# Optimization experiments

Hardware: AMD Instinct MI355X
Metric: run time of the kernel (lower is better)

Reference implementation:

```python
import jax, jax.numpy as jnp
import numpy as np

N = 50000      # nodes / stations
E = 600000     # edges
IN = 16        # in_channels
ED = 8         # edge_dim
HID = 128      # hidden
H = 4          # heads
C = HID // H   # 32 per-head channels
EMB = HID // 2 # station embedding dim
FEAT = HID - EMB
SLOPE = 0.2    # GATv2 LeakyReLU negative slope


def setup_inputs() -> dict:
    key = jax.random.key(0)
    ks = jax.random.split(key, 32)
    r = lambda i, shape, s=0.05: (jax.random.normal(ks[i], shape, jnp.float32) * s)
    inp = {
        "x": jax.random.normal(ks[0], (N, IN), jnp.float32),
        "node_idx": jax.random.randint(ks[1], (N,), 0, N),
        "edge_index": jax.random.randint(ks[2], (2, E), 0, N),
        "edge_attr": jax.random.normal(ks[3], (E, ED), jnp.float32),
        # params
        "emb": r(4, (N, EMB)),
        "W_in": r(5, (IN, FEAT)), "b_in": jnp.zeros((FEAT,), jnp.float32),
        # conv1 (GATv2: lin_l, lin_r, lin_edge, att, out bias)
        "Wl1": r(6, (HID, HID)), "bl1": jnp.zeros((HID,), jnp.float32),
        "Wr1": r(7, (HID, HID)), "br1": jnp.zeros((HID,), jnp.float32),
        "We1": r(8, (ED, HID)),  "be1": jnp.zeros((HID,), jnp.float32),
        "att1": r(9, (H, C)),    "bo1": jnp.zeros((HID,), jnp.float32),
        # conv2
        "Wl2": r(10, (HID, HID)), "bl2": jnp.zeros((HID,), jnp.float32),
        "Wr2": r(11, (HID, HID)), "br2": jnp.zeros((HID,), jnp.float32),
        "We2": r(12, (ED, HID)),  "be2": jnp.zeros((HID,), jnp.float32),
        "att2": r(13, (H, C)),    "bo2": jnp.zeros((HID,), jnp.float32),
        # layer norms
        "g1": jnp.ones((HID,), jnp.float32), "beta1": jnp.zeros((HID,), jnp.float32),
        "g2": jnp.ones((HID,), jnp.float32), "beta2": jnp.zeros((HID,), jnp.float32),
        # output head
        "W_out": r(14, (HID, 1)), "b_out": jnp.zeros((1,), jnp.float32),
    }
    return inp


def _gatv2(x, src, dst, ea, Wl, bl, Wr, br, We, be, att, bo):
    # x: [N,HID] -> per-head projections [N,H,C]
    xl = (x @ Wl + bl).reshape(-1, H, C)   # source transform
    xr = (x @ Wr + br).reshape(-1, H, C)   # target transform
    ee = (ea @ We + be).reshape(-1, H, C)  # edge transform [E,H,C]
    s = jax.nn.leaky_relu(xl[src] + xr[dst] + ee, SLOPE)  # [E,H,C]
    logit = jnp.einsum('ehc,hc->eh', s, att)              # [E,H]
    # segment softmax over destination node
    amax = jax.lax.stop_gradient(jax.ops.segment_max(logit, dst, num_segments=N))
    amax = jnp.where(jnp.isfinite(amax), amax, 0.0)
    ex = jnp.exp(logit - amax[dst])
    den = jax.ops.segment_sum(ex, dst, num_segments=N)
    alpha = ex / den[dst]                                  # [E,H]
    out = jax.ops.segment_sum(xl[src] * alpha[..., None], dst, num_segments=N)
    return out.reshape(-1, HID) + bo


def _ln(x, g, b):
    mu = x.mean(-1, keepdims=True)
    v = ((x - mu) ** 2).mean(-1, keepdims=True)
    return (x - mu) * jax.lax.rsqrt(v + 1e-5) * g + b


def reference(x, node_idx, edge_index, edge_attr, emb, W_in, b_in,
              Wl1, bl1, Wr1, br1, We1, be1, att1, bo1,
              Wl2, bl2, Wr2, br2, We2, be2, att2, bo2,
              g1, beta1, g2, beta2, W_out, b_out):
    src, dst = edge_index[0], edge_index[1]
    feat = jax.nn.relu(x @ W_in + b_in)                       # [N,FEAT]
    z = jnp.concatenate([feat, emb[node_idx]], axis=-1)       # [N,HID]
    h = jax.nn.relu(_gatv2(z, src, dst, edge_attr, Wl1, bl1, Wr1, br1, We1, be1, att1, bo1))
    z = _ln(z + h, g1, beta1)
    h = jax.nn.relu(_gatv2(z, src, dst, edge_attr, Wl2, bl2, Wr2, br2, We2, be2, att2, bo2))
    z = _ln(z + h, g2, beta2)
    return (z @ W_out + b_out).squeeze(-1)                    # [N]
```

## Files before the change

kernel.cpp:

```cpp
#include <hip/hip_runtime.h>
#include <hip/hip_bf16.h>

#define NN 50000
#define NE 600000
#define IND 16
#define EDD 8
#define HIDD 128
#define NH 4
#define CC 32
#define EMBD 64
#define FEATD 64
#define NB_SCAN ((NN + 255) / 256)
#define FILLB ((NE + 255) / 256)
#define BZB (NN / 16)
#define WPB 256
#define PRMF 896

typedef __hip_bfloat16 bf16;
typedef __attribute__((ext_vector_type(8))) short bshort8;
typedef __attribute__((ext_vector_type(4))) float floatx4;
typedef __attribute__((ext_vector_type(2))) float f32x2;

__device__ __forceinline__ unsigned short f2bu(float f) {
    unsigned int u = __float_as_uint(f);
    u += 0x7fffu + ((u >> 16) & 1u);
    return (unsigned short)(u >> 16);
}

#if defined(__has_builtin)
#if __has_builtin(__builtin_amdgcn_fdot2_f32_bf16)
#define HAS_DOT2BF 1
#endif
#endif
#ifndef HAS_DOT2BF
#define HAS_DOT2BF 0
#endif

#if HAS_DOT2BF
typedef __attribute__((ext_vector_type(2))) __bf16 bfx2;
__device__ __forceinline__ float dot2bf(unsigned int a, unsigned int b, float c) {
    return __builtin_amdgcn_fdot2_f32_bf16(__builtin_bit_cast(bfx2, a),
                                           __builtin_bit_cast(bfx2, b), c, false);
}
#else
__device__ __forceinline__ float dot2bf(unsigned int a, unsigned int b, float c) {
    float a0 = __uint_as_float(a << 16), a1 = __uint_as_float(a & 0xffff0000u);
    float b0 = __uint_as_float(b << 16), b1 = __uint_as_float(b & 0xffff0000u);
    return __builtin_fmaf(a1, b1, __builtin_fmaf(a0, b0, c));
}
#endif

template <bool F32>
__device__ __forceinline__ float LD(const void* p, long long i) {
    if constexpr (F32) return ((const float*)p)[i];
    else return __bfloat162float(((const bf16*)p)[i]);
}

__device__ __forceinline__ bool is_f32(const int* cnt) { return *cnt > 8; }

__global__ void k_detinit(const unsigned short* __restrict__ x, int nhalf,
                          int* __restrict__ cnt, int* __restrict__ deg,
                          int* __restrict__ dcnt) {
    if (blockIdx.x == 0) {
        __shared__ int red[256];
        int hits = 0;
        for (int i = threadIdx.x; i < nhalf; i += 256)
            if ((x[i] & 0x7F80u) == 0x7F80u) hits++;
        red[threadIdx.x] = hits;
        __syncthreads();
        for (int o = 128; o; o >>= 1) {
            if (threadIdx.x < o) red[threadIdx.x] += red[threadIdx.x + o];
            __syncthreads();
        }
        if (threadIdx.x == 0) *cnt = red[0];
    } else {
        int gid = (blockIdx.x - 1) * 256 + threadIdx.x;
        if (gid < NN) deg[gid] = 0;
        if (blockIdx.x == 1 && threadIdx.x < 64) dcnt[threadIdx.x] = 0;
    }
}

__global__ void k_hist(const int* __restrict__ ei, int* __restrict__ deg, int* __restrict__ rank) {
    int e = blockIdx.x * blockDim.x + threadIdx.x;
    if (e < NE) rank[e] = atomicAdd(&deg[ei[NE + e]], 1);
}

__global__ void k_scan1(const int* __restrict__ deg, int* __restrict__ off0,
                        int* __restrict__ bsum, int* __restrict__ dcnt,
                        int* __restrict__ rankd) {
    __shared__ int tile[256];
    __shared__ int lh[64];
    __shared__ int lbase[64];
    int t = threadIdx.x;
    int gid = blockIdx.x * 256 + t;
    if (t < 64) lh[t] = 0;
    __syncthreads();
    int v = (gid < NN) ? deg[gid] : 0;
    int b = 63 - min(v, 63);
    int lr = 0;
    if (gid < NN) lr = atomicAdd(&lh[b], 1);
    tile[t] = v;
    __syncthreads();
    if (t < 64) lbase[t] = lh[t] ? atomicAdd(&dcnt[t], lh[t]) : 0;
    #pragma unroll
    for (int o = 1; o < 256; o <<= 1) {
        int u = (t >= o) ? tile[t - o] : 0;
        __syncthreads();
        tile[t] += u;
        __syncthreads();
    }
    if (gid < NN) {
        off0[gid] = tile[t] - v;
        rankd[gid] = lbase[b] + lr;
    }
    if (t == 255) bsum[blockIdx.x] = tile[255];
}
__global__ void k_scan2(int* __restrict__ bsum, int* __restrict__ dcnt,
                        int* __restrict__ dbase) {
    __shared__ int tile[256];
    __shared__ int d2[64];
    int t = threadIdx.x;
    int v = (t < NB_SCAN) ? bsum[t] : 0;
    tile[t] = v;
    int dv = (t < 64) ? dcnt[t] : 0;
    if (t < 64) d2[t] = dv;
    __syncthreads();
    #pragma unroll
    for (int o = 1; o < 256; o <<= 1) {
        int u = (t >= o) ? tile[t - o] : 0;
        __syncthreads();
        tile[t] += u;
        __syncthreads();
    }
    #pragma unroll
    for (int o = 1; o < 64; o <<= 1) {
        int u = (t >= o && t < 64) ? d2[t - o] : 0;
        __syncthreads();
        if (t < 64) d2[t] += u;
        __syncthreads();
    }
    if (t < NB_SCAN) bsum[t] = tile[t] - v;
    if (t < 64) dbase[t] = d2[t] - dv;
}

template <bool F32>
__device__ void prep_impl(const int* __restrict__ off0, const int* __restrict__ bsum,
                          const int* __restrict__ deg, const int* __restrict__ rankd,
                          const int* __restrict__ dbase, int* __restrict__ perm,
                          int* __restrict__ offF,
                          const int* __restrict__ ei, const int* __restrict__ rank,
                          int* __restrict__ esrc, uint4* __restrict__ ea8, const void* ea,
                          const void* x, const int* __restrict__ node_idx, const void* emb,
                          const void* W_in, const void* b_in, bf16* __restrict__ zb,
                          const void* Wl1, const void* bl1, const void* Wr1, const void* br1,
                          const void* Wl2, const void* bl2, const void* Wr2, const void* br2,
                          bf16* __restrict__ wbT, float* __restrict__ bias,
                          const void* We1, const void* att1, const void* be1, const void* bo1,
                          const void* g1, const void* beta1,
                          const void* We2, const void* att2, const void* be2, const void* bo2,
                          const void* g2, const void* beta2,
                          const void* Wo, const void* bout,
                          unsigned int* __restrict__ wep, float* __restrict__ prm) {
    int b = blockIdx.x;
    int t = threadIdx.x;
    if (b < NB_SCAN) {
        int gid = b * 256 + t;
        if (gid < NN) {
            offF[gid] = off0[gid] + bsum[b];
            int bk = 63 - min(deg[gid], 63);
            perm[dbase[bk] + rankd[gid]] = gid;
        }
        if (gid == 0) offF[NN] = NE;
    } else if (b < NB_SCAN + FILLB) {
        int e = (b - NB_SCAN) * 256 + t;
        if (e >= NE) return;
        if (e < 16) {
            esrc[NE + e] = 0;
            uint4 z; z.x = 0; z.y = 0; z.z = 0; z.w = 0;
            ea8[NE + e] = z;
        }
        int dst = ei[NE + e];
        int slot = off0[dst] + bsum[dst >> 8] + rank[e];
        esrc[slot] = ei[e];
        uint4 v;
        if constexpr (F32) {
            const float4* ef = (const float4*)ea;
            float4 f0 = ef[2 * e], f1 = ef[2 * e + 1];
            v.x = (unsigned int)f2bu(f0.x) | ((unsigned int)f2bu(f0.y) << 16);
            v.y = (unsigned int)f2bu(f0.z) | ((unsigned int)f2bu(f0.w) << 16);
            v.z = (unsigned int)f2bu(f1.x) | ((unsigned int)f2bu(f1.y) << 16);
            v.w = (unsigned int)f2bu(f1.z) | ((unsigned int)f2bu(f1.w) << 16);
        } else {
            v = ((const uint4*)ea)[e];
        }
        ea8[slot] = v;
    } else if (b < NB_SCAN + FILLB + BZB) {
        int nb = (b - NB_SCAN - FILLB) * 16 + (t >> 7) * 8;
        int t7 = t & 127;
        if (t7 < FEATD) {
            float w[IND];
            #pragma unroll
            for (int k = 0; k < IND; k++) w[k] = LD<F32>(W_in, k * FEATD + t7);
            float bi = LD<F32>(b_in, t7);
            #pragma unroll 2
            for (int nd = 0; nd < 8; nd++) {
                int n = nb + nd;
                float acc = bi;
                #pragma unroll
                for (int k = 0; k < IND; k++)
                    acc += LD<F32>(x, (long long)n * IND + k) * w[k];
                zb[n * HIDD + t7] = __float2bfloat16(fmaxf(acc, 0.f));
            }
        } else {
            #pragma unroll 2
            for (int nd = 0; nd < 8; nd++) {
                int n = nb + nd;
                zb[n * HIDD + t7] = __float2bfloat16(
                    LD<F32>(emb, (long long)node_idx[n] * EMBD + (t7 - FEATD)));
            }
        }
    } else if (b < NB_SCAN + FILLB + BZB + WPB) {
        int bid2 = (b - NB_SCAN - FILLB - BZB) * 2 + (t >> 7);
        int layer = bid2 >> 8;
        int n2 = bid2 & 255;
        int t7 = t & 127;
        const void* W = layer ? (n2 < HIDD ? Wl2 : Wr2) : (n2 < HIDD ? Wl1 : Wr1);
        const void* bb = layer ? (n2 < HIDD ? bl2 : br2) : (n2 < HIDD ? bl1 : br1);
        int nn = n2 & (HIDD - 1);
        wbT[(layer * 256 + n2) * HIDD + t7] = __float2bfloat16(LD<F32>(W, t7 * HIDD + nn));
        if (t7 == 0) bias[layer * 256 + n2] = LD<F32>(bb, nn);
    } else {
        int layer = b - (NB_SCAN + FILLB + BZB + WPB);
        const void* We = layer ? We2 : We1;
        const void* att = layer ? att2 : att1;
        const void* be = layer ? be2 : be1;
        const void* bo = layer ? bo2 : bo1;
        const void* g  = layer ? g2 : g1;
        const void* bt = layer ? beta2 : beta1;
        if (t < 128) {
            int lane5 = t >> 2, j = t & 3, c0 = lane5 * 4;
            #pragma unroll
            for (int p = 0; p < 4; p++) {
                unsigned int lo_ = f2bu(LD<F32>(We, (2 * p) * HIDD + c0 + j));
                unsigned int hi_ = f2bu(LD<F32>(We, (2 * p + 1) * HIDD + c0 + j));
                wep[layer * 512 + lane5 * 16 + p * 4 + j] = lo_ | (hi_ << 16);
            }
        } else {
            int t2 = t - 128;
            float* Pp = prm + layer * PRMF;
            Pp[t2]        = LD<F32>(att, t2) * 1.4426950408889634f;
            Pp[128 + t2]  = LD<F32>(be, t2);
            Pp[256 + t2]  = LD<F32>(bo, t2);
            Pp[384 + t2]  = LD<F32>(g, t2);
            Pp[512 + t2]  = LD<F32>(bt, t2);
            if (layer) {
                Pp[640 + t2] = LD<F32>(Wo, t2);
                if (t2 == 0) Pp[768] = LD<F32>(bout, 0);
            }
        }
    }
}
__global__ void k_prep(const int* cnt, const int* off0, const int* bsum, const int* deg,
                       const int* rankd, const int* dbase, int* perm, int* offF,
                       const int* ei, const int* rank, int* esrc, uint4* ea8, const void* ea,
                       const void* x, const int* node_idx, const void* emb,
                       const void* W_in, const void* b_in, bf16* zb,
                       const void* Wl1, const void* bl1, const void* Wr1, const void* br1,
                       const void* Wl2, const void* bl2, const void* Wr2, const void* br2,
                       bf16* wbT, float* bias,
                       const void* We1, const void* att1, const void* be1, const void* bo1,
                       const void* g1, const void* beta1,
                       const void* We2, const void* att2, const void* be2, const void* bo2,
                       const void* g2, const void* beta2,
                       const void* Wo, const void* bout,
                       unsigned int* wep, float* prm) {
    if (is_f32(cnt))
        prep_impl<true>(off0, bsum, deg, rankd, dbase, perm, offF, ei, rank, esrc, ea8, ea,
                        x, node_idx, emb, W_in, b_in, zb, Wl1, bl1, Wr1, br1,
                        Wl2, bl2, Wr2, br2, wbT, bias, We1, att1, be1, bo1, g1, beta1,
                        We2, att2, be2, bo2, g2, beta2, Wo, bout, wep, prm);
    else
        prep_impl<false>(off0, bsum, deg, rankd, dbase, perm, offF, ei, rank, esrc, ea8, ea,
                         x, node_idx, emb, W_in, b_in, zb, Wl1, bl1, Wr1, br1,
                         Wl2, bl2, Wr2, br2, wbT, bias, We1, att1, be1, bo1, g1, beta1,
                         We2, att2, be2, bo2, g2, beta2, Wo, bout, wep, prm);
}

__global__ __launch_bounds__(256) void k_projmm(const bf16* __restrict__ zb,
                                                const bf16* __restrict__ wbT,
                                                const float* __restrict__ bias,
                                                bf16* __restrict__ xl, bf16* __restrict__ xr) {
    int wave = threadIdx.x >> 6, lane = threadIdx.x & 63;
    int n0 = wave * 64;
    int l15 = lane & 15, q = lane >> 4;
    bshort8 bfr[4][4];
    #pragma unroll
    for (int j = 0; j < 4; j++)
        #pragma unroll
        for (int s = 0; s < 4; s++)
            bfr[j][s] = *(const bshort8*)(wbT + ((n0 + j * 16 + l15) << 7) + s * 32 + q * 8);
    float bv[4];
    #pragma unroll
    for (int j = 0; j < 4; j++) bv[j] = bias[n0 + j * 16 + l15];
    #pragma unroll
    for (int mt = 0; mt < 2; mt++) {
        int m0 = blockIdx.x * 64 + mt * 32;
        const bf16* arow0 = zb + ((m0 + l15) << 7) + q * 8;
        const bf16* arow1 = arow0 + (16 << 7);
        bshort8 a0[4], a1[4];
        #pragma unroll
        for (int s = 0; s < 4; s++) a0[s] = *(const bshort8*)(arow0 + s * 32);
        #pragma unroll
        for (int s = 0; s < 4; s++) a1[s] = *(const bshort8*)(arow1 + s * 32);
        #pragma unroll
        for (int mi = 0; mi < 2; mi++) {
            floatx4 acc0 = {0.f, 0.f, 0.f, 0.f}, acc1 = acc0, acc2 = acc0, acc3 = acc0;
            #pragma unroll
            for (int s = 0; s < 4; s++) {
                bshort8 a = mi ? a1[s] : a0[s];
                acc0 = __builtin_amdgcn_mfma_f32_16x16x32_bf16(a, bfr[0][s], acc0, 0, 0, 0);
                acc1 = __builtin_amdgcn_mfma_f32_16x16x32_bf16(a, bfr[1][s], acc1, 0, 0, 0);
                acc2 = __builtin_amdgcn_mfma_f32_16x16x32_bf16(a, bfr[2][s], acc2, 0, 0, 0);
                acc3 = __builtin_amdgcn_mfma_f32_16x16x32_bf16(a, bfr[3][s], acc3, 0, 0, 0);
            }
            floatx4 accs[4] = {acc0, acc1, acc2, acc3};
            #pragma unroll
            for (int j = 0; j < 4; j++) {
                int colg = n0 + j * 16 + l15;
                bf16* dst = (colg < HIDD) ? (xl + colg) : (xr + (colg - HIDD));
                #pragma unroll
                for (int r = 0; r < 4; r++) {
                    int rowc = m0 + mi * 16 + q * 4 + r;
                    if (rowc < NN) dst[rowc << 7] = __float2bfloat16(accs[j][r] + bv[j]);
                }
            }
        }
    }
}

__device__ __forceinline__ void edge_body(uint4 eu, uint2 xu, const unsigned int (*wp)[4],
                                          const float* base, const f32x2* at2,
                                          float mask, f32x2* acc, float& den) {
    f32x2 xv0, xv1;
    xv0.x = __uint_as_float(xu.x << 16); xv0.y = __uint_as_float(xu.x & 0xffff0000u);
    xv1.x = __uint_as_float(xu.y << 16); xv1.y = __uint_as_float(xu.y & 0xffff0000u);
    f32x2 e01, e23;
    {
        float c0 = base[0];
        c0 = dot2bf(eu.x, wp[0][0], c0);
        c0 = dot2bf(eu.y, wp[1][0], c0);
        c0 = dot2bf(eu.z, wp[2][0], c0);
        c0 = dot2bf(eu.w, wp[3][0], c0);
        float c1 = base[1];
        c1 = dot2bf(eu.x, wp[0][1], c1);
        c1 = dot2bf(eu.y, wp[1][1], c1);
        c1 = dot2bf(eu.z, wp[2][1], c1);
        c1 = dot2bf(eu.w, wp[3][1], c1);
        e01.x = c0; e01.y = c1;
        float c2 = base[2];
        c2 = dot2bf(eu.x, wp[0][2], c2);
        c2 = dot2bf(eu.y, wp[1][2], c2);
        c2 = dot2bf(eu.z, wp[2][2], c2);
        c2 = dot2bf(eu.w, wp[3][2], c2);
        float c3 = base[3];
        c3 = dot2bf(eu.x, wp[0][3], c3);
        c3 = dot2bf(eu.y, wp[1][3], c3);
        c3 = dot2bf(eu.z, wp[2][3], c3);
        c3 = dot2bf(eu.w, wp[3][3], c3);
        e23.x = c2; e23.y = c3;
    }
    f32x2 s0 = xv0 + e01;
    f32x2 s1 = xv1 + e23;
    s0 = __builtin_elementwise_max(s0, s0 * 0.2f);
    s1 = __builtin_elementwise_max(s1, s1 * 0.2f);
    f32x2 lsv = s0 * at2[0] + s1 * at2[1];
    float ls = lsv.x + lsv.y;
    ls += __shfl_xor(ls, 1);
    ls += __shfl_xor(ls, 2);
    ls += __shfl_xor(ls, 4);
    float ex = exp2f(ls) * mask;
    acc[0] += ex * xv0;
    acc[1] += ex * xv1;
    den += ex;
}

template <bool LAST>
__device__ __forceinline__ void gat_impl(const int* __restrict__ perm,
                         const int* __restrict__ off, const int* __restrict__ esrc,
                         const uint4* __restrict__ ea8,
                         const unsigned int* __restrict__ wep,
                         const float* __restrict__ P,
                         const bf16* __restrict__ xl, const bf16* __restrict__ xr,
                         bf16* __restrict__ zb, void* out, bool f32out) {
    int wave = threadIdx.x >> 6;
    int half = (threadIdx.x >> 5) & 1;
    int lane5 = threadIdx.x & 31;
    int n = perm[blockIdx.x * 8 + wave * 2 + half];
    int c0 = lane5 << 2;
    unsigned int wp[4][4];
    {
        const uint4* w4 = (const uint4*)(wep + lane5 * 16);
        uint4 wa = w4[0], wb = w4[1], wc = w4[2], wd = w4[3];
        wp[0][0] = wa.x; wp[0][1] = wa.y; wp[0][2] = wa.z; wp[0][3] = wa.w;
        wp[1][0] = wb.x; wp[1][1] = wb.y; wp[1][2] = wb.z; wp[1][3] = wb.w;
        wp[2][0] = wc.x; wp[2][1] = wc.y; wp[2][2] = wc.z; wp[2][3] = wc.w;
        wp[3][0] = wd.x; wp[3][1] = wd.y; wp[3][2] = wd.z; wp[3][3] = wd.w;
    }
    float4 atv = *(const float4*)(P + c0);
    f32x2 at2[2];
    at2[0].x = atv.x; at2[0].y = atv.y;
    at2[1].x = atv.z; at2[1].y = atv.w;
    float4 bev = *(const float4*)(P + 128 + c0);
    uint2 xru = *(const uint2*)(xr + (n << 7) + c0);
    float base[4];
    base[0] = bev.x + __uint_as_float(xru.x << 16);
    base[1] = bev.y + __uint_as_float(xru.x & 0xffff0000u);
    base[2] = bev.z + __uint_as_float(xru.y << 16);
    base[3] = bev.w + __uint_as_float(xru.y & 0xffff0000u);
    int lo = off[n], hi = off[n + 1];
    f32x2 accA[2] = {{0.f, 0.f}, {0.f, 0.f}}, accB[2] = {{0.f, 0.f}, {0.f, 0.f}};
    float denA = 0.f, denB = 0.f;
    if (lo < hi) {
        int sA = esrc[lo],      sB = esrc[lo + 1];
        uint4 eA = ea8[lo],     eB = ea8[lo + 1];
        int snA = esrc[lo + 2], snB = esrc[lo + 3];
        uint4 enA = ea8[lo + 2], enB = ea8[lo + 3];
        int s2A = esrc[lo + 4], s2B = esrc[lo + 5];
        uint4 e2A = ea8[lo + 4], e2B = ea8[lo + 5];
        uint2 xA = *(const uint2*)(xl + (sA << 7) + c0);
        uint2 xB = *(const uint2*)(xl + (sB << 7) + c0);
        uint2 xnA = *(const uint2*)(xl + (snA << 7) + c0);
        uint2 xnB = *(const uint2*)(xl + (snB << 7) + c0);
        for (int i = lo; i < hi; i += 2) {
            uint2 x2A = *(const uint2*)(xl + (s2A << 7) + c0);
            uint2 x2B = *(const uint2*)(xl + (s2B << 7) + c0);
            int s3A = esrc[i + 6],  s3B = esrc[i + 7];
            uint4 e3A = ea8[i + 6], e3B = ea8[i + 7];
            edge_body(eA, xA, wp, base, at2, 1.f, accA, denA);
            float mB = (i + 1 < hi) ? 1.f : 0.f;
            edge_body(eB, xB, wp, base, at2, mB, accB, denB);
            eA = enA; enA = e2A; e2A = e3A;
            eB = enB; enB = e2B; e2B = e3B;
            xA = xnA; xnA = x2A;
            xB = xnB; xnB = x2B;
            s2A = s3A; s2B = s3B;
        }
        accA[0] += accB[0];
        accA[1] += accB[1];
        denA += denB;
    }
    float inv = (denA > 0.f) ? 1.0f / denA : 0.f;
    uint2 zu = *(const uint2*)(zb + (n << 7) + c0);
    float zv[4];
    zv[0] = __uint_as_float(zu.x << 16);
    zv[1] = __uint_as_float(zu.x & 0xffff0000u);
    zv[2] = __uint_as_float(zu.y << 16);
    zv[3] = __uint_as_float(zu.y & 0xffff0000u);
    float accf[4] = {accA[0].x, accA[0].y, accA[1].x, accA[1].y};
    float4 bo4 = *(const float4*)(P + 256 + c0);
    float bov[4] = {bo4.x, bo4.y, bo4.z, bo4.w};
    float v[4];
    float s = 0.f;
    #pragma unroll
    for (int j = 0; j < 4; j++) {
        float hv = fmaxf(accf[j] * inv + bov[j], 0.f);
        v[j] = zv[j] + hv;
        s += v[j];
    }
    #pragma unroll
    for (int m = 16; m; m >>= 1) s += __shfl_xor(s, m);
    float mu = s * (1.f / HIDD);
    float s2v = 0.f;
    float dv[4];
    #pragma unroll
    for (int j = 0; j < 4; j++) { dv[j] = v[j] - mu; s2v += dv[j] * dv[j]; }
    #pragma unroll
    for (int m = 16; m; m >>= 1) s2v += __shfl_xor(s2v, m);
    float rs = rsqrtf(s2v * (1.f / HIDD) + 1e-5f);
    float4 g4 = *(const float4*)(P + 384 + c0);
    float4 bt4 = *(const float4*)(P + 512 + c0);
    float gv[4] = {g4.x, g4.y, g4.z, g4.w};
    float btv[4] = {bt4.x, bt4.y, bt4.z, bt4.w};
    float o[4];
    #pragma unroll
    for (int j = 0; j < 4; j++)
        o[j] = dv[j] * rs * gv[j] + btv[j];
    if constexpr (!LAST) {
        uint2 pk;
        pk.x = (unsigned int)f2bu(o[0]) | ((unsigned int)f2bu(o[1]) << 16);
        pk.y = (unsigned int)f2bu(o[2]) | ((unsigned int)f2bu(o[3]) << 16);
        *(uint2*)(zb + (n << 7) + c0) = pk;
    } else {
        float4 wo4 = *(const float4*)(P + 640 + c0);
        float wov[4] = {wo4.x, wo4.y, wo4.z, wo4.w};
        float po = 0.f;
        #pragma unroll
        for (int j = 0; j < 4; j++) po += o[j] * wov[j];
        #pragma unroll
        for (int m = 16; m; m >>= 1) po += __shfl_xor(po, m);
        if (lane5 == 0) {
            float r = po + P[768];
            if (f32out) ((float*)out)[n] = r;
            else        ((bf16*)out)[n] = __float2bfloat16(r);
        }
    }
}
__global__ void k_gat(const int* perm, const int* off, const int* esrc,
                      const uint4* ea8, const unsigned int* wep, const float* prm,
                      const bf16* xl, const bf16* xr, bf16* zb) {
    gat_impl<false>(perm, off, esrc, ea8, wep, prm, xl, xr, zb, nullptr, false);
}
__global__ void k_gat_last(const int* cnt, const int* perm, const int* off, const int* esrc,
                           const uint4* ea8, const unsigned int* wep, const float* prm,
                           const bf16* xl, const bf16* xr, bf16* zb, void* out) {
    gat_impl<true>(perm, off, esrc, ea8, wep, prm, xl, xr, zb, out, is_f32(cnt));
}

extern "C" void kernel_launch(void* const* d_in, const int* in_sizes, int n_in,
                              void* d_out, int out_size, void* d_ws, size_t ws_size,
                              hipStream_t stream) {
    const void* x        = d_in[0];
    const int*  node_idx = (const int*)d_in[1];
    const int*  ei       = (const int*)d_in[2];
    const void* ea       = d_in[3];
    const void* emb      = d_in[4];
    const void* W_in     = d_in[5];
    const void* b_in     = d_in[6];
    const void* Wl1 = d_in[7];  const void* bl1 = d_in[8];
    const void* Wr1 = d_in[9];  const void* br1 = d_in[10];
    const void* We1 = d_in[11]; const void* be1 = d_in[12];
    const void* att1 = d_in[13]; const void* bo1 = d_in[14];
    const void* Wl2 = d_in[15]; const void* bl2 = d_in[16];
    const void* Wr2 = d_in[17]; const void* br2 = d_in[18];
    const void* We2 = d_in[19]; const void* be2 = d_in[20];
    const void* att2 = d_in[21]; const void* bo2 = d_in[22];
    const void* g1 = d_in[23]; const void* beta1 = d_in[24];
    const void* g2 = d_in[25]; const void* beta2 = d_in[26];
    const void* W_out = d_in[27]; const void* b_out = d_in[28];

    int*   cnt   = (int*)d_ws;
    uint4* ea8   = (uint4*)((char*)d_ws + 256);
    bf16*  zb    = (bf16*)(ea8 + NE + 16);
    bf16*  xl    = zb + NN * HIDD;
    bf16*  xr    = xl + NN * HIDD;
    bf16*  wbT   = xr + NN * HIDD;
    float* bias  = (float*)(wbT + 2 * 256 * HIDD);
    unsigned int* wep = (unsigned int*)(bias + 512);
    float* prm   = (float*)(wep + 1024);
    int*   off0  = (int*)(prm + 2 * PRMF);
    int*   offF  = off0 + NN + 1;
    int*   deg   = offF + NN + 1;
    int*   rank  = deg + NN;
    int*   rankd = rank + NE;
    int*   perm  = rankd + NN;
    int*   esrc  = perm + NN;
    int*   bsum  = esrc + NE + 16;
    int*   dcnt  = bsum + 256;
    int*   dbase = dcnt + 64;

    int nhalf = in_sizes[0] < 16384 ? in_sizes[0] : 16384;
    k_detinit<<<NB_SCAN + 1, 256, 0, stream>>>((const unsigned short*)x, nhalf, cnt, deg, dcnt);
    k_hist<<<FILLB, 256, 0, stream>>>(ei, deg, rank);
    k_scan1<<<NB_SCAN, 256, 0, stream>>>(deg, off0, bsum, dcnt, rankd);
    k_scan2<<<1, 256, 0, stream>>>(bsum, dcnt, dbase);
    k_prep<<<NB_SCAN + FILLB + BZB + WPB + 2, 256, 0, stream>>>(
        cnt, off0, bsum, deg, rankd, dbase, perm, offF, ei, rank, esrc, ea8, ea,
        x, node_idx, emb, W_in, b_in, zb,
        Wl1, bl1, Wr1, br1, Wl2, bl2, Wr2, br2, wbT, bias,
        We1, att1, be1, bo1, g1, beta1,
        We2, att2, be2, bo2, g2, beta2,
        W_out, b_out, wep, prm);

    k_projmm<<<(NN + 63) / 64, 256, 0, stream>>>(zb, wbT, bias, xl, xr);
    k_gat<<<NN / 8, 256, 0, stream>>>(perm, offF, esrc, ea8, wep, prm, xl, xr, zb);

    k_projmm<<<(NN + 63) / 64, 256, 0, stream>>>(zb, wbT + 256 * HIDD, bias + 256, xl, xr);
    k_gat_last<<<NN / 8, 256, 0, stream>>>(cnt, perm, offF, esrc, ea8, wep + 512, prm + PRMF,
                                           xl, xr, zb, d_out);
}
```

Baseline: 359.9 us.

## Fuse scan kernels, transpose projection MFMA for packed stores, deepen gather prefetch

Three separate changes. The two-pass scan becomes one kernel that uses a last-block ticket counter, which removes one launch. The projection GEMM swaps operand roles so each lane holds four consecutive output channels, letting it write packed 8-byte bf16 stores instead of scattered 2-byte ones. The GAT edge loop prefetches source indices and xl rows further ahead. The costs are more atomics and the memory-ordering risk of the ticket pattern, plus higher register pressure in the GAT loop.

```diff
diff --git a/kernel.cpp b/kernel.cpp
--- a/kernel.cpp
+++ b/kernel.cpp
@@ -76,7 +76,7 @@
     } else {
         int gid = (blockIdx.x - 1) * 256 + threadIdx.x;
         if (gid < NN) deg[gid] = 0;
-        if (blockIdx.x == 1 && threadIdx.x < 64) dcnt[threadIdx.x] = 0;
+        if (blockIdx.x == 1 && threadIdx.x < 80) dcnt[threadIdx.x] = 0;
     }
 }
 
@@ -85,12 +85,14 @@
     if (e < NE) rank[e] = atomicAdd(&deg[ei[NE + e]], 1);
 }
 
-__global__ void k_scan1(const int* __restrict__ deg, int* __restrict__ off0,
-                        int* __restrict__ bsum, int* __restrict__ dcnt,
-                        int* __restrict__ rankd) {
+__global__ void k_scan12(const int* __restrict__ deg, int* __restrict__ off0,
+                         int* __restrict__ bsum, int* __restrict__ dcnt,
+                         int* __restrict__ dbase, int* __restrict__ rankd) {
     __shared__ int tile[256];
     __shared__ int lh[64];
     __shared__ int lbase[64];
+    __shared__ int d2[64];
+    __shared__ int ticket;
     int t = threadIdx.x;
     int gid = blockIdx.x * 256 + t;
     if (t < 64) lh[t] = 0;
@@ -113,16 +115,14 @@
         off0[gid] = tile[t] - v;
         rankd[gid] = lbase[b] + lr;
     }
-    if (t == 255) bsum[blockIdx.x] = tile[255];
-}
-__global__ void k_scan2(int* __restrict__ bsum, int* __restrict__ dcnt,
-                        int* __restrict__ dbase) {
-    __shared__ int tile[256];
-    __shared__ int d2[64];
-    int t = threadIdx.x;
-    int v = (t < NB_SCAN) ? bsum[t] : 0;
-    tile[t] = v;
-    int dv = (t < 64) ? dcnt[t] : 0;
+    if (t == 255) atomicExch(&bsum[blockIdx.x], tile[255]);
+    __syncthreads();
+    if (t == 0) ticket = atomicAdd(&dcnt[64], 1);
+    __syncthreads();
+    if (ticket != NB_SCAN - 1) return;
+    int v2 = (t < NB_SCAN) ? atomicAdd(&bsum[t], 0) : 0;
+    int dv = (t < 64) ? atomicAdd(&dcnt[t], 0) : 0;
+    tile[t] = v2;
     if (t < 64) d2[t] = dv;
     __syncthreads();
     #pragma unroll
@@ -139,7 +139,7 @@
         if (t < 64) d2[t] += u;
         __syncthreads();
     }
-    if (t < NB_SCAN) bsum[t] = tile[t] - v;
+    if (t < NB_SCAN) bsum[t] = tile[t] - v2;
     if (t < 64) dbase[t] = d2[t] - dv;
 }
 
@@ -293,46 +293,44 @@
     int wave = threadIdx.x >> 6, lane = threadIdx.x & 63;
     int n0 = wave * 64;
     int l15 = lane & 15, q = lane >> 4;
-    bshort8 bfr[4][4];
+    bshort8 afr[4][4];
     #pragma unroll
     for (int j = 0; j < 4; j++)
         #pragma unroll
         for (int s = 0; s < 4; s++)
-            bfr[j][s] = *(const bshort8*)(wbT + ((n0 + j * 16 + l15) << 7) + s * 32 + q * 8);
-    float bv[4];
-    #pragma unroll
-    for (int j = 0; j < 4; j++) bv[j] = bias[n0 + j * 16 + l15];
-    #pragma unroll
-    for (int mt = 0; mt < 2; mt++) {
-        int m0 = blockIdx.x * 64 + mt * 32;
-        const bf16* arow0 = zb + ((m0 + l15) << 7) + q * 8;
-        const bf16* arow1 = arow0 + (16 << 7);
-        bshort8 a0[4], a1[4];
+            afr[j][s] = *(const bshort8*)(wbT + ((n0 + j * 16 + l15) << 7) + s * 32 + q * 8);
+    float4 bias4[4];
+    #pragma unroll
+    for (int j = 0; j < 4; j++) bias4[j] = *(const float4*)(bias + n0 + j * 16 + q * 4);
+    bf16* dst = (n0 < HIDD) ? xl : xr;
+    int cbase = (n0 & (HIDD - 1)) + q * 4;
+    int nodeBase = blockIdx.x * 64;
+    #pragma unroll
+    for (int mt = 0; mt < 4; mt++) {
+        int node = nodeBase + mt * 16 + l15;
+        const bf16* brow = zb + (node << 7) + q * 8;
+        bshort8 bfrag[4];
         #pragma unroll
-        for (int s = 0; s < 4; s++) a0[s] = *(const bshort8*)(arow0 + s * 32);
+        for (int s = 0; s < 4; s++) bfrag[s] = *(const bshort8*)(brow + s * 32);
+        floatx4 acc0 = {0.f, 0.f, 0.f, 0.f}, acc1 = acc0, acc2 = acc0, acc3 = acc0;
         #pragma unroll
-        for (int s = 0; s < 4; s++) a1[s] = *(const bshort8*)(arow1 + s * 32);
-        #pragma unroll
-        for (int mi = 0; mi < 2; mi++) {
-            floatx4 acc0 = {0.f, 0.f, 0.f, 0.f}, acc1 = acc0, acc2 = acc0, acc3 = acc0;
-            #pragma unroll
-            for (int s = 0; s < 4; s++) {
-                bshort8 a = mi ? a1[s] : a0[s];
-                acc0 = __builtin_amdgcn_mfma_f32_16x16x32_bf16(a, bfr[0][s], acc0, 0, 0, 0);
-                acc1 = __builtin_amdgcn_mfma_f32_16x16x32_bf16(a, bfr[1][s], acc1, 0, 0, 0);
-                acc2 = __builtin_amdgcn_mfma_f32_16x16x32_bf16(a, bfr[2][s], acc2, 0, 0, 0);
-                acc3 = __builtin_amdgcn_mfma_f32_16x16x32_bf16(a, bfr[3][s], acc3, 0, 0, 0);
-            }
+        for (int s = 0; s < 4; s++) {
+            acc0 = __builtin_amdgcn_mfma_f32_16x16x32_bf16(afr[0][s], bfrag[s], acc0, 0, 0, 0);
+            acc1 = __builtin_amdgcn_mfma_f32_16x16x32_bf16(afr[1][s], bfrag[s], acc1, 0, 0, 0);
+            acc2 = __builtin_amdgcn_mfma_f32_16x16x32_bf16(afr[2][s], bfrag[s], acc2, 0, 0, 0);
+            acc3 = __builtin_amdgcn_mfma_f32_16x16x32_bf16(afr[3][s], bfrag[s], acc3, 0, 0, 0);
+        }
+        if (node < NN) {
             floatx4 accs[4] = {acc0, acc1, acc2, acc3};
             #pragma unroll
             for (int j = 0; j < 4; j++) {
-                int colg = n0 + j * 16 + l15;
-                bf16* dst = (colg < HIDD) ? (xl + colg) : (xr + (colg - HIDD));
-                #pragma unroll
-                for (int r = 0; r < 4; r++) {
-                    int rowc = m0 + mi * 16 + q * 4 + r;
-                    if (rowc < NN) dst[rowc << 7] = __float2bfloat16(accs[j][r] + bv[j]);
-                }
+                float4 bv = bias4[j];
+                uint2 pk;
+                pk.x = (unsigned int)f2bu(accs[j][0] + bv.x) |
+                       ((unsigned int)f2bu(accs[j][1] + bv.y) << 16);
+                pk.y = (unsigned int)f2bu(accs[j][2] + bv.z) |
+                       ((unsigned int)f2bu(accs[j][3] + bv.w) << 16);
+                *(uint2*)(dst + (node << 7) + cbase + j * 16) = pk;
             }
         }
     }
@@ -422,28 +420,33 @@
     float denA = 0.f, denB = 0.f;
     if (lo < hi) {
         int sA = esrc[lo],      sB = esrc[lo + 1];
-        uint4 eA = ea8[lo],     eB = ea8[lo + 1];
         int snA = esrc[lo + 2], snB = esrc[lo + 3];
+        int s2A = esrc[lo + 4], s2B = esrc[lo + 5];
+        int s6A = esrc[lo + 6], s6B = esrc[lo + 7];
+        int s8A = esrc[lo + 8], s8B = esrc[lo + 9];
+        uint4 eA = ea8[lo],      eB = ea8[lo + 1];
         uint4 enA = ea8[lo + 2], enB = ea8[lo + 3];
-        int s2A = esrc[lo + 4], s2B = esrc[lo + 5];
         uint4 e2A = ea8[lo + 4], e2B = ea8[lo + 5];
-        uint2 xA = *(const uint2*)(xl + (sA << 7) + c0);
-        uint2 xB = *(const uint2*)(xl + (sB << 7) + c0);
+        uint2 xA  = *(const uint2*)(xl + (sA << 7) + c0);
+        uint2 xB  = *(const uint2*)(xl + (sB << 7) + c0);
         uint2 xnA = *(const uint2*)(xl + (snA << 7) + c0);
         uint2 xnB = *(const uint2*)(xl + (snB << 7) + c0);
+        uint2 x2A = *(const uint2*)(xl + (s2A << 7) + c0);
+        uint2 x2B = *(const uint2*)(xl + (s2B << 7) + c0);
         for (int i = lo; i < hi; i += 2) {
-            uint2 x2A = *(const uint2*)(xl + (s2A << 7) + c0);
-            uint2 x2B = *(const uint2*)(xl + (s2B << 7) + c0);
-            int s3A = esrc[i + 6],  s3B = esrc[i + 7];
+            uint2 x3A = *(const uint2*)(xl + (s6A << 7) + c0);
+            uint2 x3B = *(const uint2*)(xl + (s6B << 7) + c0);
             uint4 e3A = ea8[i + 6], e3B = ea8[i + 7];
+            int s10A = esrc[i + 10], s10B = esrc[i + 11];
             edge_body(eA, xA, wp, base, at2, 1.f, accA, denA);
             float mB = (i + 1 < hi) ? 1.f : 0.f;
             edge_body(eB, xB, wp, base, at2, mB, accB, denB);
             eA = enA; enA = e2A; e2A = e3A;
             eB = enB; enB = e2B; e2B = e3B;
-            xA = xnA; xnA = x2A;
-            xB = xnB; xnB = x2B;
-            s2A = s3A; s2B = s3B;
+            xA = xnA; xnA = x2A; x2A = x3A;
+            xB = xnB; xnB = x2B; x2B = x3B;
+            s6A = s8A; s8A = s10A;
+            s6B = s8B; s8B = s10B;
         }
         accA[0] += accB[0];
         accA[1] += accB[1];
@@ -556,13 +559,12 @@
     int*   esrc  = perm + NN;
     int*   bsum  = esrc + NE + 16;
     int*   dcnt  = bsum + 256;
-    int*   dbase = dcnt + 64;
+    int*   dbase = dcnt + 80;
 
     int nhalf = in_sizes[0] < 16384 ? in_sizes[0] : 16384;
     k_detinit<<<NB_SCAN + 1, 256, 0, stream>>>((const unsigned short*)x, nhalf, cnt, deg, dcnt);
     k_hist<<<FILLB, 256, 0, stream>>>(ei, deg, rank);
-    k_scan1<<<NB_SCAN, 256, 0, stream>>>(deg, off0, bsum, dcnt, rankd);
-    k_scan2<<<1, 256, 0, stream>>>(bsum, dcnt, dbase);
+    k_scan12<<<NB_SCAN, 256, 0, stream>>>(deg, off0, bsum, dcnt, dbase, rankd);
     k_prep<<<NB_SCAN + FILLB + BZB + WPB + 2, 256, 0, stream>>>(
         cnt, off0, bsum, deg, rankd, dbase, perm, offF, ei, rank, esrc, ea8, ea,
         x, node_idx, emb, W_in, b_in, zb,
```

Measured after the change: 349.7 us. 1.03x faster.
